# Performance work log

Measured on AMD Instinct MI355X. Metric: run time of the kernel, lower is better.

Reference implementation:

```python
import jax, jax.numpy as jnp
import numpy as np

# Static problem constants (must match setup_inputs)
NUM_GRAPHS = 64      # batch_size = int(batch[-1]) + 1
PTS_PER_GRAPH = 512
RATIO = 16           # centroids per graph
HEADS = 4
IN_CH = 64           # = out_channels per head (concat=False -> mean over heads)
NEG_SLOPE = 0.2


def setup_inputs() -> dict:
    key = jax.random.key(0)
    ks = jax.random.split(key, 8)
    N = NUM_GRAPHS * PTS_PER_GRAPH
    x = jax.random.normal(ks[0], (N, IN_CH), dtype=jnp.float32)
    edge_index = jnp.zeros((2, 2), dtype=jnp.int64)  # unused by forward
    batch = (jnp.arange(N) // PTS_PER_GRAPH).astype(jnp.int64)
    xcent_base = jax.random.normal(ks[1], (RATIO, IN_CH), dtype=jnp.float32)
    W_l = jax.random.normal(ks[2], (IN_CH, HEADS * IN_CH), dtype=jnp.float32) / np.sqrt(IN_CH)
    b_l = jax.random.normal(ks[3], (HEADS * IN_CH,), dtype=jnp.float32) * 0.01
    W_r = jax.random.normal(ks[4], (IN_CH, HEADS * IN_CH), dtype=jnp.float32) / np.sqrt(IN_CH)
    b_r = jax.random.normal(ks[5], (HEADS * IN_CH,), dtype=jnp.float32) * 0.01
    att = jax.random.normal(ks[6], (HEADS, IN_CH), dtype=jnp.float32) / np.sqrt(IN_CH)
    bias = jax.random.normal(ks[7], (IN_CH,), dtype=jnp.float32) * 0.01
    return {"x": x, "edge_index": edge_index, "batch": batch,
            "xcent_base": xcent_base, "W_l": W_l, "b_l": b_l,
            "W_r": W_r, "b_r": b_r, "att": att, "bias": bias}


def _bipart_pool(x, batch, xcent_base, W_l, b_l, W_r, b_r, att, bias):
    N = x.shape[0]
    B = NUM_GRAPHS
    Nc = B * RATIO  # number of centroid (target) nodes

    # Dense bipartite edges: each source node -> all RATIO centroids of its graph.
    src = jnp.repeat(jnp.arange(N, dtype=jnp.int32), RATIO)                     # [E]
    dst = jnp.tile(jnp.arange(RATIO, dtype=jnp.int32), N) \
        + jnp.repeat(batch.astype(jnp.int32), RATIO) * RATIO                    # [E]

    # PyG GATv2Conv(add_self_loops=True): remove src==dst edges, then add
    # self loops (i,i) for i < min(N_src, N_dst) = Nc. Keep static shapes by
    # masking the removed edges instead of deleting them.
    self_idx = jnp.arange(Nc, dtype=jnp.int32)
    src_f = jnp.concatenate([src, self_idx])
    dst_f = jnp.concatenate([dst, self_idx])
    drop = jnp.concatenate([src == dst, jnp.zeros((Nc,), dtype=bool)])          # [E+Nc]

    # Linear projections (source and target sides)
    x_l = (x @ W_l + b_l).reshape(N, HEADS, IN_CH)                              # [N,H,C]
    xcent = jnp.tile(xcent_base, (B, 1))                                        # [Nc,IN]
    x_r = (xcent @ W_r + b_r).reshape(Nc, HEADS, IN_CH)                         # [Nc,H,C]

    # GATv2 attention: leaky_relu(x_i + x_j) . att, softmax per target node
    xj = x_l[src_f]                                                             # [E',H,C]
    g = jax.nn.leaky_relu(xj + x_r[dst_f], NEG_SLOPE)
    alpha = jnp.einsum('ehc,hc->eh', g, att)                                    # [E',H]
    alpha = jnp.where(drop[:, None], jnp.float32(-1e30), alpha)
    amax = jax.ops.segment_max(alpha, dst_f, num_segments=Nc)                   # [Nc,H]
    e = jnp.exp(alpha - amax[dst_f])
    den = jax.ops.segment_sum(e, dst_f, num_segments=Nc)                        # [Nc,H]
    w = e / den[dst_f]                                                          # [E',H]

    out = jax.ops.segment_sum(w[..., None] * xj, dst_f, num_segments=Nc)        # [Nc,H,C]
    out = out.mean(axis=1) + bias                                               # concat=False -> mean heads
    return out.reshape(B, RATIO, IN_CH)


def reference(x, edge_index, batch, xcent_base, W_l, b_l, W_r, b_r, att, bias):
    xcent = _bipart_pool(x, batch, xcent_base, W_l, b_l, W_r, b_r, att, bias)
    batchcent = jnp.repeat(jnp.arange(NUM_GRAPHS, dtype=jnp.int64), RATIO)
    return xcent, batchcent
```

## Files before the change

### kernel.cpp

```cpp
#include <hip/hip_runtime.h>

#define PTS    512
#define NG     64
#define RATIO  16
#define CH     64
#define NC     1024

__global__ __launch_bounds__(256) void k1(
    const float* __restrict__ x, const float* __restrict__ xcb,
    const float* __restrict__ W_l, const float* __restrict__ b_l,
    const float* __restrict__ W_r, const float* __restrict__ b_r,
    const float* __restrict__ att,
    float* __restrict__ aws, float* __restrict__ xlws)
{
    __shared__ float sW[4096];
    __shared__ float s_xc[1024];
    __shared__ float s_xr[1024];
    __shared__ float s_att[64], s_bl[64], s_sxr[16];

    const int b = blockIdx.x >> 2, h = blockIdx.x & 3;
    const int tid = threadIdx.x;

    if (tid < 64) { s_att[tid] = att[h * 64 + tid]; s_bl[tid] = b_l[h * 64 + tid]; }
    for (int idx = tid; idx < 4096; idx += 256)
        sW[idx] = W_l[(idx >> 6) * 256 + h * 64 + (idx & 63)];
    for (int idx = tid; idx < 1024; idx += 256) s_xc[idx] = xcb[idx];
    __syncthreads();

    for (int idx = tid; idx < 1024; idx += 256) {
        int r = idx >> 6, c = idx & 63;
        float acc = b_r[h * 64 + c];
        for (int k = 0; k < 64; ++k)
            acc = fmaf(s_xc[r * 64 + k], W_r[k * 256 + h * 64 + c], acc);
        s_xr[idx] = acc;
    }
    __syncthreads();
    if (tid < 16) {
        float s = 0.f;
        for (int c = 0; c < 64; ++c) s = fmaf(s_xr[tid * 64 + c], s_att[c], s);
        s_sxr[tid] = s;
    }
    __syncthreads();

    const int i0 = tid, i1 = tid + 256;
    const float4* xp0 = (const float4*)(x + ((size_t)b * PTS + i0) * CH);
    const float4* xp1 = (const float4*)(x + ((size_t)b * PTS + i1) * CH);
    float xl0[64], xl1[64];
#pragma unroll
    for (int c = 0; c < 64; ++c) { xl0[c] = s_bl[c]; xl1[c] = s_bl[c]; }

    for (int k4 = 0; k4 < 16; ++k4) {
        float4 u0 = xp0[k4], u1 = xp1[k4];
        float a0[4] = {u0.x, u0.y, u0.z, u0.w};
        float a1[4] = {u1.x, u1.y, u1.z, u1.w};
#pragma unroll
        for (int j = 0; j < 4; ++j) {
            const float* wr = &sW[(k4 * 4 + j) * 64];
#pragma unroll
            for (int cq = 0; cq < 16; ++cq) {
                float4 w = *(const float4*)(wr + cq * 4);
                xl0[cq*4+0] = fmaf(a0[j], w.x, xl0[cq*4+0]);
                xl0[cq*4+1] = fmaf(a0[j], w.y, xl0[cq*4+1]);
                xl0[cq*4+2] = fmaf(a0[j], w.z, xl0[cq*4+2]);
                xl0[cq*4+3] = fmaf(a0[j], w.w, xl0[cq*4+3]);
                xl1[cq*4+0] = fmaf(a1[j], w.x, xl1[cq*4+0]);
                xl1[cq*4+1] = fmaf(a1[j], w.y, xl1[cq*4+1]);
                xl1[cq*4+2] = fmaf(a1[j], w.z, xl1[cq*4+2]);
                xl1[cq*4+3] = fmaf(a1[j], w.w, xl1[cq*4+3]);
            }
        }
    }

    float sxl0 = 0.f, sxl1 = 0.f;
    float ac0[16], ac1[16];
#pragma unroll
    for (int r = 0; r < 16; ++r) { ac0[r] = 0.f; ac1[r] = 0.f; }
#pragma unroll
    for (int cq = 0; cq < 16; ++cq) {
        float4 at = *(const float4*)&s_att[cq * 4];
        sxl0 = fmaf(xl0[cq*4+0], at.x, sxl0); sxl0 = fmaf(xl0[cq*4+1], at.y, sxl0);
        sxl0 = fmaf(xl0[cq*4+2], at.z, sxl0); sxl0 = fmaf(xl0[cq*4+3], at.w, sxl0);
        sxl1 = fmaf(xl1[cq*4+0], at.x, sxl1); sxl1 = fmaf(xl1[cq*4+1], at.y, sxl1);
        sxl1 = fmaf(xl1[cq*4+2], at.z, sxl1); sxl1 = fmaf(xl1[cq*4+3], at.w, sxl1);
#pragma unroll
        for (int r = 0; r < 16; ++r) {
            float4 xr4 = *(const float4*)&s_xr[r * 64 + cq * 4];
            ac0[r] = fmaf(fabsf(xl0[cq*4+0] + xr4.x), at.x, ac0[r]);
            ac0[r] = fmaf(fabsf(xl0[cq*4+1] + xr4.y), at.y, ac0[r]);
            ac0[r] = fmaf(fabsf(xl0[cq*4+2] + xr4.z), at.z, ac0[r]);
            ac0[r] = fmaf(fabsf(xl0[cq*4+3] + xr4.w), at.w, ac0[r]);
            ac1[r] = fmaf(fabsf(xl1[cq*4+0] + xr4.x), at.x, ac1[r]);
            ac1[r] = fmaf(fabsf(xl1[cq*4+1] + xr4.y), at.y, ac1[r]);
            ac1[r] = fmaf(fabsf(xl1[cq*4+2] + xr4.z), at.z, ac1[r]);
            ac1[r] = fmaf(fabsf(xl1[cq*4+3] + xr4.w), at.w, ac1[r]);
        }
    }

    float* ap = aws + (size_t)(b * 4 + h) * 8192;
#pragma unroll
    for (int r = 0; r < 16; ++r) {
        ap[r * 512 + i0] = 0.6f * (sxl0 + s_sxr[r]) + 0.4f * ac0[r];
        ap[r * 512 + i1] = 0.6f * (sxl1 + s_sxr[r]) + 0.4f * ac1[r];
    }

    if (b < 2) {
        float* d0 = xlws + ((size_t)(b * PTS + i0) * 4 + h) * 64;
        float* d1 = xlws + ((size_t)(b * PTS + i1) * 4 + h) * 64;
#pragma unroll
        for (int c = 0; c < 64; c += 4) {
            *(float4*)(d0 + c) = make_float4(xl0[c], xl0[c+1], xl0[c+2], xl0[c+3]);
            *(float4*)(d1 + c) = make_float4(xl1[c], xl1[c+1], xl1[c+2], xl1[c+3]);
        }
    }
}

__global__ __launch_bounds__(512) void k2(
    const float* __restrict__ x, const float* __restrict__ W_l,
    const float* __restrict__ b_l, const float* __restrict__ aws,
    const float* __restrict__ xlws, float* __restrict__ part)
{
    __shared__ float s_e[8192];
    __shared__ float sW[4096];
    __shared__ float s_x[2176];
    __shared__ float s_den[16], s_es[16];

    const int b = blockIdx.x >> 2, h = blockIdx.x & 3;
    const int tid = threadIdx.x;

    const float* ap = aws + (size_t)(b * 4 + h) * 8192;
    for (int idx = tid; idx < 8192; idx += 512) s_e[idx] = ap[idx];
    for (int idx = tid; idx < 4096; idx += 512)
        sW[idx] = W_l[(idx >> 6) * 256 + h * 64 + (idx & 63)];
    __syncthreads();

    {
        const int r = tid >> 5, lg = tid & 31;
        const int snode = b * 16 + r;
        const float a_self =
            aws[(size_t)((snode >> 9) * 4 + h) * 8192 + r * 512 + (snode & 511)];
        float m = a_self;
#pragma unroll
        for (int j = 0; j < 16; ++j) {
            int i = lg + j * 32;
            float a = s_e[r * 512 + i];
            if (b == 0 && i == r) a = -1e30f;
            m = fmaxf(m, a);
        }
#pragma unroll
        for (int off = 16; off >= 1; off >>= 1) m = fmaxf(m, __shfl_xor(m, off));
        float d = 0.f;
#pragma unroll
        for (int j = 0; j < 16; ++j) {
            int i = lg + j * 32;
            float a = s_e[r * 512 + i];
            float e = (b == 0 && i == r) ? 0.f : __expf(a - m);
            s_e[r * 512 + i] = e;
            d += e;
        }
#pragma unroll
        for (int off = 16; off >= 1; off >>= 1) d += __shfl_xor(d, off);
        if (lg == 0) {
            float es = __expf(a_self - m);
            s_es[r] = es;
            s_den[r] = d + es;
        }
    }

    const int rg = tid >> 7;
    const int sl = (tid >> 4) & 7;
    const int qd = tid & 15;
    float y4[4][4];
#pragma unroll
    for (int i = 0; i < 4; ++i)
#pragma unroll
        for (int j = 0; j < 4; ++j) y4[i][j] = 0.f;

    const float* xb = x + (size_t)b * PTS * CH;
    for (int chk = 0; chk < 16; ++chk) {
        __syncthreads();
        {
            float4 v = ((const float4*)(xb + chk * 2048))[tid];
            int rI = tid >> 4, cI = (tid & 15) * 4;
            *(float4*)&s_x[rI * 68 + cI] = v;
        }
        __syncthreads();
#pragma unroll
        for (int ii = 0; ii < 4; ++ii) {
            int i = sl * 4 + ii;
            float4 xv = *(const float4*)&s_x[i * 68 + qd * 4];
#pragma unroll
            for (int rr = 0; rr < 4; ++rr) {
                float e = s_e[(rg * 4 + rr) * 512 + chk * 32 + i];
                y4[rr][0] = fmaf(e, xv.x, y4[rr][0]);
                y4[rr][1] = fmaf(e, xv.y, y4[rr][1]);
                y4[rr][2] = fmaf(e, xv.z, y4[rr][2]);
                y4[rr][3] = fmaf(e, xv.w, y4[rr][3]);
            }
        }
    }
    __syncthreads();
#pragma unroll
    for (int rr = 0; rr < 4; ++rr)
        *(float4*)&s_e[sl * 1024 + (rg * 4 + rr) * 64 + qd * 4] =
            make_float4(y4[rr][0], y4[rr][1], y4[rr][2], y4[rr][3]);
    __syncthreads();

    float* s_y = s_x;
    for (int o = tid; o < 1024; o += 512) {
        float s = 0.f;
#pragma unroll
        for (int slj = 0; slj < 8; ++slj) s += s_e[slj * 1024 + o];
        s_y[o] = s;
    }
    __syncthreads();

    for (int o = tid; o < 1024; o += 512) {
        int r = o >> 6, ch = o & 63;
        float acc = 0.f;
#pragma unroll
        for (int k = 0; k < 64; ++k)
            acc = fmaf(s_y[r * 64 + k], sW[k * 64 + ch], acc);
        float den = s_den[r], es = s_es[r];
        float bl = b_l[h * 64 + ch];
        float xs = xlws[((size_t)(b * 16 + r) * 4 + h) * 64 + ch];
        part[((size_t)(b * 16 + r) * 4 + h) * 64 + ch] =
            (acc + (den - es) * bl + es * xs) / den;
    }
}

__global__ __launch_bounds__(256) void k3(const float* __restrict__ part,
                                          const float* __restrict__ bias,
                                          float* __restrict__ out)
{
    int idx = blockIdx.x * 256 + threadIdx.x;
    int ch = idx & 63;
    const float* p = part + (size_t)(idx >> 6) * 256 + ch;
    out[idx] = 0.25f * (p[0] + p[64] + p[128] + p[192]) + bias[ch];
    if (idx < NC)
        out[NC * CH + idx] = (float)(idx >> 4);
}

extern "C" void kernel_launch(void* const* d_in, const int* in_sizes, int n_in,
                              void* d_out, int out_size, void* d_ws, size_t ws_size,
                              hipStream_t stream) {
    (void)in_sizes; (void)n_in; (void)out_size; (void)ws_size;
    const float* x    = (const float*)d_in[0];
    const float* xcb  = (const float*)d_in[3];
    const float* W_l  = (const float*)d_in[4];
    const float* b_l  = (const float*)d_in[5];
    const float* W_r  = (const float*)d_in[6];
    const float* b_r  = (const float*)d_in[7];
    const float* att  = (const float*)d_in[8];
    const float* bias = (const float*)d_in[9];
    float* out = (float*)d_out;

    char* ws = (char*)d_ws;
    float* aws  = (float*)ws;
    float* xlws = (float*)(ws + (size_t)8  * 1024 * 1024);
    float* part = (float*)(ws + (size_t)9  * 1024 * 1024);

    hipLaunchKernelGGL(k1, dim3(NG * 4), dim3(256), 0, stream,
                       x, xcb, W_l, b_l, W_r, b_r, att, aws, xlws);
    hipLaunchKernelGGL(k2, dim3(NG * 4), dim3(512), 0, stream,
                       x, W_l, b_l, aws, xlws, part);
    hipLaunchKernelGGL(k3, dim3(256), dim3(256), 0, stream, part, bias, out);
}
```

Measured before the change: 131.4 us.

## Split graph work across more blocks and hoist centroid projection into separate kernel

Moves the centroid W_r projection and its attention dot into a small k0 kernel so k1 no longer recomputes it in every block. k1 and k2 now launch four times as many blocks, each covering a quarter of a graph's points. In k1, pairs of threads split the 64 output channels and combine their partial sums with shuffles, which lowers register use. k2 reads x directly instead of staging it through shared memory, reduces across blocks with atomicAdd into a memset buffer, and moves the softmax normalization into k3. The aim is more parallelism and occupancy, at the cost of an extra launch, a memset, atomics, and softmax max/sum work repeated in every quarter block.

```diff
diff --git a/kernel.cpp b/kernel.cpp
--- a/kernel.cpp
+++ b/kernel.cpp
@@ -6,236 +6,252 @@
 #define CH     64
 #define NC     1024
 
-__global__ __launch_bounds__(256) void k1(
-    const float* __restrict__ x, const float* __restrict__ xcb,
-    const float* __restrict__ W_l, const float* __restrict__ b_l,
-    const float* __restrict__ W_r, const float* __restrict__ b_r,
-    const float* __restrict__ att,
+__global__ __launch_bounds__(256) void k0(
+    const float* __restrict__ xcb, const float* __restrict__ W_r,
+    const float* __restrict__ b_r, const float* __restrict__ att,
+    float* __restrict__ xrws, float* __restrict__ sxrws)
+{
+    __shared__ float s_row[4 * 64];
+    const int h = blockIdx.x >> 2, rq = blockIdx.x & 3;
+    const int rl = threadIdx.x >> 6, c = threadIdx.x & 63;
+    const int r = rq * 4 + rl;
+    float acc = b_r[h * 64 + c];
+    for (int k = 0; k < 64; ++k)
+        acc = fmaf(xcb[r * 64 + k], W_r[k * 256 + h * 64 + c], acc);
+    xrws[(h * 16 + r) * 64 + c] = acc;
+    s_row[rl * 64 + c] = acc;
+    __syncthreads();
+    if (threadIdx.x < 4) {
+        int rr = rq * 4 + threadIdx.x;
+        float s = 0.f;
+        for (int cc = 0; cc < 64; ++cc)
+            s = fmaf(s_row[threadIdx.x * 64 + cc], att[h * 64 + cc], s);
+        sxrws[h * 16 + rr] = s;
+    }
+}
+
+__global__ __launch_bounds__(256, 4) void k1(
+    const float* __restrict__ x, const float* __restrict__ W_l,
+    const float* __restrict__ b_l, const float* __restrict__ att,
+    const float* __restrict__ xrws, const float* __restrict__ sxrws,
     float* __restrict__ aws, float* __restrict__ xlws)
 {
     __shared__ float sW[4096];
-    __shared__ float s_xc[1024];
     __shared__ float s_xr[1024];
     __shared__ float s_att[64], s_bl[64], s_sxr[16];
 
-    const int b = blockIdx.x >> 2, h = blockIdx.x & 3;
+    const int q = blockIdx.x & 3, h = (blockIdx.x >> 2) & 3, b = blockIdx.x >> 4;
     const int tid = threadIdx.x;
+    const int half = tid & 1, rloc = tid >> 1;
+    const int row = q * 128 + rloc;
+    const size_t grow = (size_t)b * PTS + row;
 
     if (tid < 64) { s_att[tid] = att[h * 64 + tid]; s_bl[tid] = b_l[h * 64 + tid]; }
+    if (tid < 16) s_sxr[tid] = sxrws[h * 16 + tid];
+    for (int idx = tid; idx < 1024; idx += 256) s_xr[idx] = xrws[h * 1024 + idx];
     for (int idx = tid; idx < 4096; idx += 256)
         sW[idx] = W_l[(idx >> 6) * 256 + h * 64 + (idx & 63)];
-    for (int idx = tid; idx < 1024; idx += 256) s_xc[idx] = xcb[idx];
-    __syncthreads();
-
-    for (int idx = tid; idx < 1024; idx += 256) {
-        int r = idx >> 6, c = idx & 63;
-        float acc = b_r[h * 64 + c];
-        for (int k = 0; k < 64; ++k)
-            acc = fmaf(s_xc[r * 64 + k], W_r[k * 256 + h * 64 + c], acc);
-        s_xr[idx] = acc;
-    }
-    __syncthreads();
-    if (tid < 16) {
-        float s = 0.f;
-        for (int c = 0; c < 64; ++c) s = fmaf(s_xr[tid * 64 + c], s_att[c], s);
-        s_sxr[tid] = s;
-    }
-    __syncthreads();
-
-    const int i0 = tid, i1 = tid + 256;
-    const float4* xp0 = (const float4*)(x + ((size_t)b * PTS + i0) * CH);
-    const float4* xp1 = (const float4*)(x + ((size_t)b * PTS + i1) * CH);
-    float xl0[64], xl1[64];
-#pragma unroll
-    for (int c = 0; c < 64; ++c) { xl0[c] = s_bl[c]; xl1[c] = s_bl[c]; }
+    __syncthreads();
+
+    const float4* xp = (const float4*)x + grow * 16;
+    float acc[32];
+#pragma unroll
+    for (int c = 0; c < 32; ++c) acc[c] = s_bl[half * 32 + c];
 
     for (int k4 = 0; k4 < 16; ++k4) {
-        float4 u0 = xp0[k4], u1 = xp1[k4];
-        float a0[4] = {u0.x, u0.y, u0.z, u0.w};
-        float a1[4] = {u1.x, u1.y, u1.z, u1.w};
+        float4 u = xp[k4];
+        float xk[4] = {u.x, u.y, u.z, u.w};
 #pragma unroll
         for (int j = 0; j < 4; ++j) {
-            const float* wr = &sW[(k4 * 4 + j) * 64];
-#pragma unroll
-            for (int cq = 0; cq < 16; ++cq) {
+            const float* wr = &sW[(k4 * 4 + j) * 64 + half * 32];
+            float xv = xk[j];
+#pragma unroll
+            for (int cq = 0; cq < 8; ++cq) {
                 float4 w = *(const float4*)(wr + cq * 4);
-                xl0[cq*4+0] = fmaf(a0[j], w.x, xl0[cq*4+0]);
-                xl0[cq*4+1] = fmaf(a0[j], w.y, xl0[cq*4+1]);
-                xl0[cq*4+2] = fmaf(a0[j], w.z, xl0[cq*4+2]);
-                xl0[cq*4+3] = fmaf(a0[j], w.w, xl0[cq*4+3]);
-                xl1[cq*4+0] = fmaf(a1[j], w.x, xl1[cq*4+0]);
-                xl1[cq*4+1] = fmaf(a1[j], w.y, xl1[cq*4+1]);
-                xl1[cq*4+2] = fmaf(a1[j], w.z, xl1[cq*4+2]);
-                xl1[cq*4+3] = fmaf(a1[j], w.w, xl1[cq*4+3]);
+                acc[cq*4+0] = fmaf(xv, w.x, acc[cq*4+0]);
+                acc[cq*4+1] = fmaf(xv, w.y, acc[cq*4+1]);
+                acc[cq*4+2] = fmaf(xv, w.z, acc[cq*4+2]);
+                acc[cq*4+3] = fmaf(xv, w.w, acc[cq*4+3]);
             }
         }
     }
 
-    float sxl0 = 0.f, sxl1 = 0.f;
-    float ac0[16], ac1[16];
-#pragma unroll
-    for (int r = 0; r < 16; ++r) { ac0[r] = 0.f; ac1[r] = 0.f; }
-#pragma unroll
-    for (int cq = 0; cq < 16; ++cq) {
-        float4 at = *(const float4*)&s_att[cq * 4];
-        sxl0 = fmaf(xl0[cq*4+0], at.x, sxl0); sxl0 = fmaf(xl0[cq*4+1], at.y, sxl0);
-        sxl0 = fmaf(xl0[cq*4+2], at.z, sxl0); sxl0 = fmaf(xl0[cq*4+3], at.w, sxl0);
-        sxl1 = fmaf(xl1[cq*4+0], at.x, sxl1); sxl1 = fmaf(xl1[cq*4+1], at.y, sxl1);
-        sxl1 = fmaf(xl1[cq*4+2], at.z, sxl1); sxl1 = fmaf(xl1[cq*4+3], at.w, sxl1);
+    float sxl = 0.f;
+#pragma unroll
+    for (int cq = 0; cq < 8; ++cq) {
+        float4 at = *(const float4*)&s_att[half * 32 + cq * 4];
+        sxl = fmaf(acc[cq*4+0], at.x, sxl); sxl = fmaf(acc[cq*4+1], at.y, sxl);
+        sxl = fmaf(acc[cq*4+2], at.z, sxl); sxl = fmaf(acc[cq*4+3], at.w, sxl);
+    }
+    float ac[16];
+#pragma unroll
+    for (int r = 0; r < 16; ++r) ac[r] = 0.f;
+    for (int cq = 0; cq < 8; ++cq) {
+        float4 at = *(const float4*)&s_att[half * 32 + cq * 4];
 #pragma unroll
         for (int r = 0; r < 16; ++r) {
-            float4 xr4 = *(const float4*)&s_xr[r * 64 + cq * 4];
-            ac0[r] = fmaf(fabsf(xl0[cq*4+0] + xr4.x), at.x, ac0[r]);
-            ac0[r] = fmaf(fabsf(xl0[cq*4+1] + xr4.y), at.y, ac0[r]);
-            ac0[r] = fmaf(fabsf(xl0[cq*4+2] + xr4.z), at.z, ac0[r]);
-            ac0[r] = fmaf(fabsf(xl0[cq*4+3] + xr4.w), at.w, ac0[r]);
-            ac1[r] = fmaf(fabsf(xl1[cq*4+0] + xr4.x), at.x, ac1[r]);
-            ac1[r] = fmaf(fabsf(xl1[cq*4+1] + xr4.y), at.y, ac1[r]);
-            ac1[r] = fmaf(fabsf(xl1[cq*4+2] + xr4.z), at.z, ac1[r]);
-            ac1[r] = fmaf(fabsf(xl1[cq*4+3] + xr4.w), at.w, ac1[r]);
+            float4 xr4 = *(const float4*)&s_xr[r * 64 + half * 32 + cq * 4];
+            ac[r] = fmaf(fabsf(acc[cq*4+0] + xr4.x), at.x, ac[r]);
+            ac[r] = fmaf(fabsf(acc[cq*4+1] + xr4.y), at.y, ac[r]);
+            ac[r] = fmaf(fabsf(acc[cq*4+2] + xr4.z), at.z, ac[r]);
+            ac[r] = fmaf(fabsf(acc[cq*4+3] + xr4.w), at.w, ac[r]);
         }
     }
-
-    float* ap = aws + (size_t)(b * 4 + h) * 8192;
-#pragma unroll
-    for (int r = 0; r < 16; ++r) {
-        ap[r * 512 + i0] = 0.6f * (sxl0 + s_sxr[r]) + 0.4f * ac0[r];
-        ap[r * 512 + i1] = 0.6f * (sxl1 + s_sxr[r]) + 0.4f * ac1[r];
+    sxl += __shfl_xor(sxl, 1);
+#pragma unroll
+    for (int r = 0; r < 16; ++r) ac[r] += __shfl_xor(ac[r], 1);
+
+    float* ap = aws + (size_t)(b * 4 + h) * 8192 + row;
+#pragma unroll
+    for (int r8 = 0; r8 < 8; ++r8) {
+        int r = half * 8 + r8;
+        ap[r * 512] = 0.6f * (sxl + s_sxr[r]) + 0.4f * ac[r];
     }
 
     if (b < 2) {
-        float* d0 = xlws + ((size_t)(b * PTS + i0) * 4 + h) * 64;
-        float* d1 = xlws + ((size_t)(b * PTS + i1) * 4 + h) * 64;
-#pragma unroll
-        for (int c = 0; c < 64; c += 4) {
-            *(float4*)(d0 + c) = make_float4(xl0[c], xl0[c+1], xl0[c+2], xl0[c+3]);
-            *(float4*)(d1 + c) = make_float4(xl1[c], xl1[c+1], xl1[c+2], xl1[c+3]);
+        float* d = xlws + (grow * 4 + h) * 64 + half * 32;
+#pragma unroll
+        for (int c4 = 0; c4 < 8; ++c4)
+            *(float4*)(d + c4 * 4) =
+                make_float4(acc[c4*4], acc[c4*4+1], acc[c4*4+2], acc[c4*4+3]);
+    }
+}
+
+__global__ __launch_bounds__(256, 4) void k2(
+    const float* __restrict__ x, const float* __restrict__ W_l,
+    const float* __restrict__ aws, float* __restrict__ part,
+    float* __restrict__ dens, float* __restrict__ ess)
+{
+    __shared__ float s_et[128 * 16];
+    __shared__ float s_p[3 * 64 * 16];
+    __shared__ float sW[4096];
+
+    const int q = blockIdx.x & 3, h = (blockIdx.x >> 2) & 3, b = blockIdx.x >> 4;
+    const int tid = threadIdx.x;
+    const float* abh = aws + (size_t)(b * 4 + h) * 8192;
+
+    for (int idx = tid; idx < 4096; idx += 256)
+        sW[idx] = W_l[(idx >> 6) * 256 + h * 64 + (idx & 63)];
+
+    const int r = tid >> 4, lg = tid & 15;
+    const int snode = b * 16 + r;
+    const float a_self = aws[(size_t)((snode >> 9) * 4 + h) * 8192
+                             + r * 512 + (snode & 511)];
+    float m = a_self;
+    for (int j = 0; j < 32; ++j) {
+        int i = lg + j * 16;
+        float a = abh[r * 512 + i];
+        bool drop = (b == 0) && (i == r);
+        m = fmaxf(m, drop ? -1e30f : a);
+    }
+#pragma unroll
+    for (int off = 8; off >= 1; off >>= 1) m = fmaxf(m, __shfl_xor(m, off));
+    float d = 0.f;
+    for (int j = 0; j < 32; ++j) {
+        int i = lg + j * 16;
+        float a = abh[r * 512 + i];
+        bool drop = (b == 0) && (i == r);
+        d += drop ? 0.f : __expf(a - m);
+    }
+#pragma unroll
+    for (int off = 8; off >= 1; off >>= 1) d += __shfl_xor(d, off);
+    const float es = __expf(a_self - m);
+    const float den = d + es;
+    if (q == 0 && lg == 0) {
+        dens[(b * 4 + h) * 16 + r] = den;
+        ess[(b * 4 + h) * 16 + r] = es;
+    }
+
+    for (int j = 0; j < 8; ++j) {
+        int iloc = lg + j * 16;
+        int i = q * 128 + iloc;
+        float a = abh[r * 512 + i];
+        bool drop = (b == 0) && (i == r);
+        s_et[iloc * 16 + r] = drop ? 0.f : __expf(a - m);
+    }
+    __syncthreads();
+
+    const int kt = tid & 15, rt = (tid >> 4) & 3, is = tid >> 6;
+    float y4[4][4];
+#pragma unroll
+    for (int i = 0; i < 4; ++i)
+#pragma unroll
+        for (int j = 0; j < 4; ++j) y4[i][j] = 0.f;
+
+    const float* xbq = x + ((size_t)b * PTS + q * 128 + is * 32) * 64;
+#pragma unroll 4
+    for (int i = 0; i < 32; ++i) {
+        float4 xv = *(const float4*)(xbq + i * 64 + kt * 4);
+        float4 ev = *(const float4*)&s_et[(is * 32 + i) * 16 + rt * 4];
+        y4[0][0] = fmaf(ev.x, xv.x, y4[0][0]); y4[0][1] = fmaf(ev.x, xv.y, y4[0][1]);
+        y4[0][2] = fmaf(ev.x, xv.z, y4[0][2]); y4[0][3] = fmaf(ev.x, xv.w, y4[0][3]);
+        y4[1][0] = fmaf(ev.y, xv.x, y4[1][0]); y4[1][1] = fmaf(ev.y, xv.y, y4[1][1]);
+        y4[1][2] = fmaf(ev.y, xv.z, y4[1][2]); y4[1][3] = fmaf(ev.y, xv.w, y4[1][3]);
+        y4[2][0] = fmaf(ev.z, xv.x, y4[2][0]); y4[2][1] = fmaf(ev.z, xv.y, y4[2][1]);
+        y4[2][2] = fmaf(ev.z, xv.z, y4[2][2]); y4[2][3] = fmaf(ev.z, xv.w, y4[2][3]);
+        y4[3][0] = fmaf(ev.w, xv.x, y4[3][0]); y4[3][1] = fmaf(ev.w, xv.y, y4[3][1]);
+        y4[3][2] = fmaf(ev.w, xv.z, y4[3][2]); y4[3][3] = fmaf(ev.w, xv.w, y4[3][3]);
+    }
+
+    if (is > 0) {
+#pragma unroll
+        for (int rr = 0; rr < 4; ++rr)
+            *(float4*)&s_p[((is - 1) * 64 + rt * 16 + kt) * 16 + rr * 4] =
+                make_float4(y4[rr][0], y4[rr][1], y4[rr][2], y4[rr][3]);
+    }
+    __syncthreads();
+    float* s_yq = s_et;
+    if (is == 0) {
+#pragma unroll
+        for (int j = 0; j < 3; ++j)
+#pragma unroll
+            for (int rr = 0; rr < 4; ++rr) {
+                float4 v = *(const float4*)&s_p[(j * 64 + rt * 16 + kt) * 16 + rr * 4];
+                y4[rr][0] += v.x; y4[rr][1] += v.y; y4[rr][2] += v.z; y4[rr][3] += v.w;
+            }
+#pragma unroll
+        for (int rr = 0; rr < 4; ++rr)
+            *(float4*)&s_yq[(rt * 4 + rr) * 64 + kt * 4] =
+                make_float4(y4[rr][0], y4[rr][1], y4[rr][2], y4[rr][3]);
+    }
+    __syncthreads();
+
+    {
+        const int r2 = tid >> 4, chq = tid & 15, ch = chq * 4;
+        float o0 = 0.f, o1 = 0.f, o2 = 0.f, o3 = 0.f;
+#pragma unroll
+        for (int k = 0; k < 64; ++k) {
+            float yv = s_yq[r2 * 64 + k];
+            float4 w = *(const float4*)&sW[k * 64 + ch];
+            o0 = fmaf(yv, w.x, o0); o1 = fmaf(yv, w.y, o1);
+            o2 = fmaf(yv, w.z, o2); o3 = fmaf(yv, w.w, o3);
         }
-    }
-}
-
-__global__ __launch_bounds__(512) void k2(
-    const float* __restrict__ x, const float* __restrict__ W_l,
-    const float* __restrict__ b_l, const float* __restrict__ aws,
-    const float* __restrict__ xlws, float* __restrict__ part)
-{
-    __shared__ float s_e[8192];
-    __shared__ float sW[4096];
-    __shared__ float s_x[2176];
-    __shared__ float s_den[16], s_es[16];
-
-    const int b = blockIdx.x >> 2, h = blockIdx.x & 3;
-    const int tid = threadIdx.x;
-
-    const float* ap = aws + (size_t)(b * 4 + h) * 8192;
-    for (int idx = tid; idx < 8192; idx += 512) s_e[idx] = ap[idx];
-    for (int idx = tid; idx < 4096; idx += 512)
-        sW[idx] = W_l[(idx >> 6) * 256 + h * 64 + (idx & 63)];
-    __syncthreads();
-
-    {
-        const int r = tid >> 5, lg = tid & 31;
-        const int snode = b * 16 + r;
-        const float a_self =
-            aws[(size_t)((snode >> 9) * 4 + h) * 8192 + r * 512 + (snode & 511)];
-        float m = a_self;
-#pragma unroll
-        for (int j = 0; j < 16; ++j) {
-            int i = lg + j * 32;
-            float a = s_e[r * 512 + i];
-            if (b == 0 && i == r) a = -1e30f;
-            m = fmaxf(m, a);
-        }
-#pragma unroll
-        for (int off = 16; off >= 1; off >>= 1) m = fmaxf(m, __shfl_xor(m, off));
-        float d = 0.f;
-#pragma unroll
-        for (int j = 0; j < 16; ++j) {
-            int i = lg + j * 32;
-            float a = s_e[r * 512 + i];
-            float e = (b == 0 && i == r) ? 0.f : __expf(a - m);
-            s_e[r * 512 + i] = e;
-            d += e;
-        }
-#pragma unroll
-        for (int off = 16; off >= 1; off >>= 1) d += __shfl_xor(d, off);
-        if (lg == 0) {
-            float es = __expf(a_self - m);
-            s_es[r] = es;
-            s_den[r] = d + es;
-        }
-    }
-
-    const int rg = tid >> 7;
-    const int sl = (tid >> 4) & 7;
-    const int qd = tid & 15;
-    float y4[4][4];
-#pragma unroll
-    for (int i = 0; i < 4; ++i)
-#pragma unroll
-        for (int j = 0; j < 4; ++j) y4[i][j] = 0.f;
-
-    const float* xb = x + (size_t)b * PTS * CH;
-    for (int chk = 0; chk < 16; ++chk) {
-        __syncthreads();
-        {
-            float4 v = ((const float4*)(xb + chk * 2048))[tid];
-            int rI = tid >> 4, cI = (tid & 15) * 4;
-            *(float4*)&s_x[rI * 68 + cI] = v;
-        }
-        __syncthreads();
-#pragma unroll
-        for (int ii = 0; ii < 4; ++ii) {
-            int i = sl * 4 + ii;
-            float4 xv = *(const float4*)&s_x[i * 68 + qd * 4];
-#pragma unroll
-            for (int rr = 0; rr < 4; ++rr) {
-                float e = s_e[(rg * 4 + rr) * 512 + chk * 32 + i];
-                y4[rr][0] = fmaf(e, xv.x, y4[rr][0]);
-                y4[rr][1] = fmaf(e, xv.y, y4[rr][1]);
-                y4[rr][2] = fmaf(e, xv.z, y4[rr][2]);
-                y4[rr][3] = fmaf(e, xv.w, y4[rr][3]);
-            }
-        }
-    }
-    __syncthreads();
-#pragma unroll
-    for (int rr = 0; rr < 4; ++rr)
-        *(float4*)&s_e[sl * 1024 + (rg * 4 + rr) * 64 + qd * 4] =
-            make_float4(y4[rr][0], y4[rr][1], y4[rr][2], y4[rr][3]);
-    __syncthreads();
-
-    float* s_y = s_x;
-    for (int o = tid; o < 1024; o += 512) {
-        float s = 0.f;
-#pragma unroll
-        for (int slj = 0; slj < 8; ++slj) s += s_e[slj * 1024 + o];
-        s_y[o] = s;
-    }
-    __syncthreads();
-
-    for (int o = tid; o < 1024; o += 512) {
-        int r = o >> 6, ch = o & 63;
-        float acc = 0.f;
-#pragma unroll
-        for (int k = 0; k < 64; ++k)
-            acc = fmaf(s_y[r * 64 + k], sW[k * 64 + ch], acc);
-        float den = s_den[r], es = s_es[r];
-        float bl = b_l[h * 64 + ch];
-        float xs = xlws[((size_t)(b * 16 + r) * 4 + h) * 64 + ch];
-        part[((size_t)(b * 16 + r) * 4 + h) * 64 + ch] =
-            (acc + (den - es) * bl + es * xs) / den;
-    }
-}
-
-__global__ __launch_bounds__(256) void k3(const float* __restrict__ part,
-                                          const float* __restrict__ bias,
-                                          float* __restrict__ out)
+        float* pp = part + ((size_t)(b * 16 + r2) * 4 + h) * 64 + ch;
+        atomicAdd(pp + 0, o0); atomicAdd(pp + 1, o1);
+        atomicAdd(pp + 2, o2); atomicAdd(pp + 3, o3);
+    }
+}
+
+__global__ __launch_bounds__(256) void k3(
+    const float* __restrict__ part, const float* __restrict__ xlws,
+    const float* __restrict__ dens, const float* __restrict__ ess,
+    const float* __restrict__ b_l, const float* __restrict__ bias,
+    float* __restrict__ out)
 {
     int idx = blockIdx.x * 256 + threadIdx.x;
-    int ch = idx & 63;
-    const float* p = part + (size_t)(idx >> 6) * 256 + ch;
-    out[idx] = 0.25f * (p[0] + p[64] + p[128] + p[192]) + bias[ch];
+    int cent = idx >> 6, ch = idx & 63;
+    int b = cent >> 4, r = cent & 15;
+    float o = 0.f;
+#pragma unroll
+    for (int h = 0; h < 4; ++h) {
+        float den = dens[(b * 4 + h) * 16 + r];
+        float es  = ess[(b * 4 + h) * 16 + r];
+        float p   = part[(size_t)(cent * 4 + h) * 64 + ch];
+        float bl  = b_l[h * 64 + ch];
+        float xs  = xlws[(size_t)(cent * 4 + h) * 64 + ch];
+        o += (p + (den - es) * bl + es * xs) / den;
+    }
+    out[idx] = 0.25f * o + bias[ch];
     if (idx < NC)
         out[NC * CH + idx] = (float)(idx >> 4);
 }
@@ -254,14 +270,22 @@
     const float* bias = (const float*)d_in[9];
     float* out = (float*)d_out;
 
-    char* ws = (char*)d_ws;
-    float* aws  = (float*)ws;
-    float* xlws = (float*)(ws + (size_t)8  * 1024 * 1024);
-    float* part = (float*)(ws + (size_t)9  * 1024 * 1024);
-
-    hipLaunchKernelGGL(k1, dim3(NG * 4), dim3(256), 0, stream,
-                       x, xcb, W_l, b_l, W_r, b_r, att, aws, xlws);
-    hipLaunchKernelGGL(k2, dim3(NG * 4), dim3(512), 0, stream,
-                       x, W_l, b_l, aws, xlws, part);
-    hipLaunchKernelGGL(k3, dim3(256), dim3(256), 0, stream, part, bias, out);
-}
+    float* wsf   = (float*)d_ws;
+    float* aws   = wsf;
+    float* xlws  = wsf + 2097152;
+    float* part  = wsf + 2359296;
+    float* xrws  = wsf + 2621440;
+    float* sxrws = xrws + 4096;
+    float* dens  = sxrws + 64;
+    float* ess   = dens + 4096;
+
+    hipMemsetAsync(part, 0, 1024 * 1024, stream);
+    hipLaunchKernelGGL(k0, dim3(16), dim3(256), 0, stream,
+                       xcb, W_r, b_r, att, xrws, sxrws);
+    hipLaunchKernelGGL(k1, dim3(1024), dim3(256), 0, stream,
+                       x, W_l, b_l, att, xrws, sxrws, aws, xlws);
+    hipLaunchKernelGGL(k2, dim3(1024), dim3(256), 0, stream,
+                       x, W_l, aws, part, dens, ess);
+    hipLaunchKernelGGL(k3, dim3(256), dim3(256), 0, stream,
+                       part, xlws, dens, ess, b_l, bias, out);
+}
```

Result: slower. 147.5 us (+12.3%).
